# Kernel optimization log

Measured on AMD Instinct MI355X. Metric: run time of the kernel, lower is better.

The kernel has to match this reference:

```python
import jax, jax.numpy as jnp
import numpy as np

IN_DIM = 1024
EMBED = 1024
HEADS = 16
HEAD_DIM = EMBED // HEADS
MAX_LEN = 401


def _sinusoidal_pe(max_len, d_model):
    pos = np.arange(max_len, dtype=np.float32)[:, None]
    div = np.exp(np.arange(0, d_model, 2, dtype=np.float32) * (-np.log(10000.0) / d_model))
    pe = np.zeros((max_len, d_model), dtype=np.float32)
    pe[:, 0::2] = np.sin(pos * div)
    pe[:, 1::2] = np.cos(pos * div)
    return jnp.asarray(pe[None])  # [1, max_len, d]


def setup_inputs() -> dict:
    key = jax.random.key(0)
    ks = jax.random.split(key, 16)
    B, S = 32, 400
    s = 1.0 / np.sqrt(IN_DIM)
    inp = {
        "query": jax.random.normal(ks[0], (B, S, IN_DIM), jnp.float32),
        "key": jax.random.normal(ks[1], (B, S, IN_DIM), jnp.float32),
        "value": jax.random.normal(ks[2], (B, S, IN_DIM), jnp.float32),
        "attn_mask": jnp.zeros((S, S), jnp.float32),
        "pe": _sinusoidal_pe(MAX_LEN, IN_DIM),
        "Wq": jax.random.normal(ks[3], (EMBED, IN_DIM), jnp.float32) * s,
        "bq": jax.random.normal(ks[4], (EMBED,), jnp.float32) * s,
        "Wk": jax.random.normal(ks[5], (EMBED, IN_DIM), jnp.float32) * s,
        "bk": jax.random.normal(ks[6], (EMBED,), jnp.float32) * s,
        "Wv": jax.random.normal(ks[7], (EMBED, IN_DIM), jnp.float32) * s,
        "bv": jax.random.normal(ks[8], (EMBED,), jnp.float32) * s,
        "Wp": jax.random.normal(ks[9], (EMBED, IN_DIM), jnp.float32) * s,
        "bp": jax.random.normal(ks[10], (EMBED,), jnp.float32) * s,
        "Wo": jax.random.normal(ks[11], (IN_DIM, EMBED), jnp.float32) / np.sqrt(EMBED),
        "bo": jax.random.normal(ks[12], (IN_DIM,), jnp.float32) / np.sqrt(EMBED),
        "gates": jax.random.normal(ks[13], (1,), jnp.float32),
    }
    return inp


def reference(query, key, value, attn_mask, pe, Wq, bq, Wk, bk, Wv, bv, Wp, bp, Wo, bo, gates):
    B, Sq, _ = query.shape
    Sk = key.shape[1]
    H, D = HEADS, HEAD_DIM

    pos_q = pe[:, :Sq] @ Wp.T + bp   # [1, Sq, E]
    pos_k = pe[:, :Sk] @ Wp.T + bp   # [1, Sk, E]

    q = (query @ Wq.T + bq + pos_q).reshape(B, Sq, H, D).transpose(0, 2, 1, 3)
    k = (key @ Wk.T + bk + pos_k).reshape(B, Sk, H, D).transpose(0, 2, 1, 3)
    v = (value @ Wv.T + bv + pos_k).reshape(B, Sk, H, D).transpose(0, 2, 1, 3)

    scores = jnp.einsum('bhqd,bhkd->bhqk', q, k) / jnp.sqrt(jnp.float32(D))
    scores = scores + attn_mask[None, None]  # additive mask broadcast over batch/heads
    attn = jax.nn.softmax(scores, axis=-1)   # dropout p=0.0 -> identity

    out = jnp.einsum('bhqk,bhkd->bhqd', attn, v)
    out = out.transpose(0, 2, 1, 3).reshape(B, Sq, H * D)
    return (out @ Wo.T + bo) * gates
```

## Files before the change

kernel.cpp:

```cpp
#include <hip/hip_runtime.h>

typedef __bf16 bf16;
typedef __bf16 bf16x8 __attribute__((ext_vector_type(8)));
typedef __bf16 bf16x4 __attribute__((ext_vector_type(4)));
typedef float f32x4 __attribute__((ext_vector_type(4)));

#define MFMA(a, b, c) __builtin_amdgcn_mfma_f32_16x16x32_bf16(a, b, c, 0, 0, 0)

__device__ __forceinline__ void g2l16(void* lds, const void* g) {
  __builtin_amdgcn_global_load_lds(
      (const __attribute__((address_space(1))) void*)g,
      (__attribute__((address_space(3))) void*)lds, 16, 0, 0);
}

__global__ void cvt_all(
    const float* __restrict__ Wq, const float* __restrict__ Wk, const float* __restrict__ Wv,
    const float* __restrict__ Wo, const float* __restrict__ Wp, const float* __restrict__ pe,
    const float* __restrict__ Xq, const float* __restrict__ Xk, const float* __restrict__ Xv,
    bf16* __restrict__ wqb, bf16* __restrict__ wkb, bf16* __restrict__ wvb,
    bf16* __restrict__ wob, bf16* __restrict__ wpb, bf16* __restrict__ peb,
    bf16* __restrict__ xqb, bf16* __restrict__ xkb, bf16* __restrict__ xvb) {
  int b = blockIdx.x;
  const float* s;
  bf16* d;
  int lb;
  if (b < 5120) {
    int t = b >> 10;
    lb = b & 1023;
    s = (t == 0) ? Wq : (t == 1) ? Wk : (t == 2) ? Wv : (t == 3) ? Wo : Wp;
    d = (t == 0) ? wqb : (t == 1) ? wkb : (t == 2) ? wvb : (t == 3) ? wob : wpb;
  } else if (b < 5520) {
    lb = b - 5120;
    s = pe;
    d = peb;
  } else {
    int bb = b - 5520;
    int t = bb / 12800;
    lb = bb - t * 12800;
    s = (t == 0) ? Xq : (t == 1) ? Xk : Xv;
    d = (t == 0) ? xqb : (t == 1) ? xkb : xvb;
  }
  int i = lb * 256 + threadIdx.x;
  f32x4 v = *(const f32x4*)(s + (size_t)i * 4);
  bf16x4 o;
  o[0] = (bf16)v[0]; o[1] = (bf16)v[1]; o[2] = (bf16)v[2]; o[3] = (bf16)v[3];
  *(bf16x4*)(d + (size_t)i * 4) = o;
}

__global__ __launch_bounds__(256) void gemm_pos(
    const bf16* __restrict__ peb, const bf16* __restrict__ Wpb,
    const float* __restrict__ bp, const float* __restrict__ bq,
    const float* __restrict__ bk, const float* __restrict__ bv,
    bf16* __restrict__ posq, bf16* __restrict__ posk, bf16* __restrict__ posv) {
  __shared__ bf16 smA[128 * 32];
  __shared__ bf16 smB[128 * 32];
  const int mbase = blockIdx.y * 128;
  const int nbase = blockIdx.x * 128;
  const int tid = threadIdx.x;
  const int lane = tid & 63, w = tid >> 6;
  const int wm = (w >> 1) * 64, wn = (w & 1) * 64;
  const int lrow = lane & 15, kg = lane >> 4;
  const f32x4 fz = {0.f, 0.f, 0.f, 0.f};
  f32x4 acc[4][4];
#pragma unroll
  for (int i = 0; i < 4; ++i)
#pragma unroll
    for (int j = 0; j < 4; ++j) acc[i][j] = fz;

  for (int k0 = 0; k0 < 1024; k0 += 32) {
    __syncthreads();
#pragma unroll
    for (int it = 0; it < 2; ++it) {
      int j = it * 256 + tid;
      int r = j >> 2, cl = j & 3;
      int c = cl ^ ((r >> 1) & 3);
      if (mbase + r < 400)
        g2l16(smA + j * 8, peb + (mbase + r) * 1024 + k0 + c * 8);
      else {
        uint4 zz = make_uint4(0, 0, 0, 0);
        *(uint4*)(smA + j * 8) = zz;
      }
    }
#pragma unroll
    for (int it = 0; it < 2; ++it) {
      int j = it * 256 + tid;
      int r = j >> 2, cl = j & 3;
      int c = cl ^ ((r >> 1) & 3);
      g2l16(smB + j * 8, Wpb + (nbase + r) * 1024 + k0 + c * 8);
    }
    __syncthreads();
    bf16x8 af[4], bfr[4];
#pragma unroll
    for (int mt = 0; mt < 4; ++mt) {
      int r = wm + mt * 16 + lrow;
      int ch = kg ^ ((r >> 1) & 3);
      af[mt] = *(const bf16x8*)(smA + r * 32 + ch * 8);
    }
#pragma unroll
    for (int nt = 0; nt < 4; ++nt) {
      int r = wn + nt * 16 + lrow;
      int ch = kg ^ ((r >> 1) & 3);
      bfr[nt] = *(const bf16x8*)(smB + r * 32 + ch * 8);
    }
#pragma unroll
    for (int nt = 0; nt < 4; ++nt)
#pragma unroll
      for (int mt = 0; mt < 4; ++mt)
        acc[mt][nt] = MFMA(af[mt], bfr[nt], acc[mt][nt]);
  }
#pragma unroll
  for (int mt = 0; mt < 4; ++mt)
#pragma unroll
    for (int rg = 0; rg < 4; ++rg) {
      int m = mbase + wm + mt * 16 + kg * 4 + rg;
      if (m < 400) {
#pragma unroll
        for (int nt = 0; nt < 4; ++nt) {
          int n = nbase + wn + nt * 16 + lrow;
          float base = acc[mt][nt][rg] + bp[n];
          posq[m * 1024 + n] = (bf16)(base + bq[n]);
          posk[m * 1024 + n] = (bf16)(base + bk[n]);
          posv[m * 1024 + n] = (bf16)(base + bv[n]);
        }
      }
    }
}

__global__ __launch_bounds__(512, 4) void gemm_qkv(
    const bf16* __restrict__ Xqb, const bf16* __restrict__ Xkb, const bf16* __restrict__ Xvb,
    const bf16* __restrict__ Wqb, const bf16* __restrict__ Wkb, const bf16* __restrict__ Wvb,
    const bf16* __restrict__ posq, const bf16* __restrict__ posk, const bf16* __restrict__ posv,
    bf16* __restrict__ qb, bf16* __restrict__ kbuf, bf16* __restrict__ vt) {
  const int lid = blockIdx.x;
  const int mI = ((lid >> 6) << 3) + (lid & 7);
  const int nI = (lid >> 3) & 7;
  if (mI >= 100) return;
  __shared__ bf16 sm[16384];
  bf16* smA = sm;
  bf16* smB = sm + 8192;
  const int z = blockIdx.y;
  const bf16* X = (z == 0) ? Xqb : (z == 1) ? Xkb : Xvb;
  const bf16* W = (z == 0) ? Wqb : (z == 1) ? Wkb : Wvb;
  const bf16* posz = (z == 0) ? posq : (z == 1) ? posk : posv;
  const int mbase = mI * 128;
  const int nbase = nI * 128;
  const int tid = threadIdx.x;
  const int lane = tid & 63, w = tid >> 6;
  const int wm = (w >> 1) * 32, wn = (w & 1) * 64;
  const int lrow = lane & 15, kg = lane >> 4;
  const f32x4 fz = {0.f, 0.f, 0.f, 0.f};
  f32x4 acc[2][4];
#pragma unroll
  for (int i = 0; i < 2; ++i)
#pragma unroll
    for (int j = 0; j < 4; ++j) acc[i][j] = fz;

  for (int k0 = 0; k0 < 1024; k0 += 64) {
    __syncthreads();
#pragma unroll
    for (int it = 0; it < 2; ++it) {
      int j = it * 512 + tid;
      int r = j >> 3, cl = j & 7;
      g2l16(smA + j * 8, X + (size_t)(mbase + r) * 1024 + k0 + (cl ^ (r & 7)) * 8);
    }
#pragma unroll
    for (int it = 0; it < 2; ++it) {
      int j = it * 512 + tid;
      int r = j >> 3, cl = j & 7;
      g2l16(smB + j * 8, W + (size_t)(nbase + r) * 1024 + k0 + (cl ^ (r & 7)) * 8);
    }
    __syncthreads();
#pragma unroll
    for (int ks = 0; ks < 2; ++ks) {
      bf16x8 af[2], bfr[4];
#pragma unroll
      for (int mt = 0; mt < 2; ++mt) {
        int r = wm + mt * 16 + lrow;
        af[mt] = *(const bf16x8*)(smA + r * 64 + ((ks * 4 + kg) ^ (r & 7)) * 8);
      }
#pragma unroll
      for (int nt = 0; nt < 4; ++nt) {
        int r = wn + nt * 16 + lrow;
        bfr[nt] = *(const bf16x8*)(smB + r * 64 + ((ks * 4 + kg) ^ (r & 7)) * 8);
      }
#pragma unroll
      for (int nt = 0; nt < 4; ++nt)
#pragma unroll
        for (int mt = 0; mt < 2; ++mt)
          acc[mt][nt] = MFMA(af[mt], bfr[nt], acc[mt][nt]);
    }
  }

  if (z < 2) {
    bf16* dst = (z == 0) ? qb : kbuf;
#pragma unroll
    for (int mt = 0; mt < 2; ++mt)
#pragma unroll
      for (int rg = 0; rg < 4; ++rg) {
        int m = mbase + wm + mt * 16 + kg * 4 + rg;
        int bI = m / 400;
        int s = m - bI * 400;
#pragma unroll
        for (int nt = 0; nt < 4; ++nt) {
          int n = nbase + wn + nt * 16 + lrow;
          float v = acc[mt][nt][rg] + (float)posz[s * 1024 + n];
          int h = n >> 6, d = n & 63;
          dst[((size_t)(bI * 16 + h) * 400 + s) * 64 + d] = (bf16)v;
        }
      }
  } else {
    __syncthreads();
    bf16* T = sm;
#pragma unroll
    for (int nt = 0; nt < 4; ++nt) {
      int n = wn + nt * 16 + lrow;
      int ng = nbase + n;
#pragma unroll
      for (int mt = 0; mt < 2; ++mt) {
        int m0 = wm + mt * 16 + kg * 4;
        bf16x4 v4;
#pragma unroll
        for (int rg = 0; rg < 4; ++rg) {
          int m = mbase + m0 + rg;
          int bI = m / 400;
          int s = m - bI * 400;
          v4[rg] = (bf16)(acc[mt][nt][rg] + (float)posz[s * 1024 + ng]);
        }
        int chk = m0 >> 3;
        int st = chk ^ (n & 15);
        *(bf16x4*)(T + n * 128 + st * 8 + (m0 & 7)) = v4;
      }
    }
    __syncthreads();
#pragma unroll
    for (int p = 0; p < 4; ++p) {
      int n = p * 32 + (tid >> 4);
      int chk = tid & 15;
      bf16x8 row = *(const bf16x8*)(T + n * 128 + (chk ^ (n & 15)) * 8);
      int ng = nbase + n;
      int h = ng >> 6, d = ng & 63;
      int m = mbase + chk * 8;
      int bI = m / 400;
      int s = m - bI * 400;
      *(bf16x8*)(vt + ((size_t)(bI * 16 + h) * 64 + d) * 400 + s) = row;
    }
  }
}

__global__ __launch_bounds__(512, 4) void attn_kernel(
    const bf16* __restrict__ qg, const bf16* __restrict__ kg_,
    const bf16* __restrict__ vg, const float* __restrict__ mask,
    bf16* __restrict__ ao) {
  const int lid = blockIdx.x;
  const int qt = (lid >> 3) & 3;
  const int bh = ((lid >> 5) << 3) + (lid & 7);
  __shared__ bf16 smQ[128 * 64];
  __shared__ bf16 smK[128 * 64];
  __shared__ bf16 smV[64 * 128];
  __shared__ bf16 smP[128 * 128];
  const int qbase = qt * 128;
  const int tid = threadIdx.x;
  const int lane = tid & 63;
  const int w = tid >> 6;
  const int lrow = lane & 15, kg = lane >> 4;
  const bf16* Qg = qg + bh * 25600;
  const bf16* Kg = kg_ + bh * 25600;
  const bf16* Vg = vg + bh * 25600;

#pragma unroll
  for (int it = 0; it < 2; ++it) {
    int j = it * 512 + tid;
    int r = j >> 3, cl = j & 7;
    int c = cl ^ (r & 7);
    int s = qbase + r;
    uint4 val = make_uint4(0, 0, 0, 0);
    if (s < 400) val = *(const uint4*)(Qg + s * 64 + c * 8);
    *(uint4*)(smQ + j * 8) = val;
  }

  const f32x4 fz = {0.f, 0.f, 0.f, 0.f};
  f32x4 o[4];
#pragma unroll
  for (int i = 0; i < 4; ++i) o[i] = fz;
  float m_run[4], l_run[4];
  const float* mrow4[4];
#pragma unroll
  for (int i = 0; i < 4; ++i) {
    m_run[i] = -1e30f;
    l_run[i] = 0.f;
    int qs = qbase + w * 16 + kg * 4 + i;
    mrow4[i] = mask + (size_t)((qs < 400) ? qs : 399) * 400;
  }

  for (int kt = 0; kt < 3; ++kt) {
#pragma unroll
    for (int it = 0; it < 2; ++it) {
      int j = it * 512 + tid;
      int r = j >> 3, cl = j & 7;
      int c = cl ^ (r & 7);
      *(uint4*)(smK + j * 8) = *(const uint4*)(Kg + (kt * 128 + r) * 64 + c * 8);
    }
#pragma unroll
    for (int it = 0; it < 2; ++it) {
      int j = it * 512 + tid;
      int r = j >> 4, cl = j & 15;
      int c = cl ^ (r & 15);
      *(uint4*)(smV + j * 8) = *(const uint4*)(Vg + r * 400 + kt * 128 + c * 8);
    }
    __syncthreads();

    f32x4 sc[8];
#pragma unroll
    for (int nt = 0; nt < 8; ++nt) sc[nt] = fz;
    __builtin_amdgcn_s_setprio(1);
#pragma unroll
    for (int ks = 0; ks < 2; ++ks) {
      int rq = w * 16 + lrow;
      int chq = (ks * 4 + kg) ^ (rq & 7);
      bf16x8 aq = *(const bf16x8*)(smQ + rq * 64 + chq * 8);
#pragma unroll
      for (int nt = 0; nt < 8; ++nt) {
        int rk2 = nt * 16 + lrow;
        int chk = (ks * 4 + kg) ^ (rk2 & 7);
        bf16x8 bk8 = *(const bf16x8*)(smK + rk2 * 64 + chk * 8);
        sc[nt] = MFMA(aq, bk8, sc[nt]);
      }
    }
    __builtin_amdgcn_s_setprio(0);

    float alpha[4];
#pragma unroll
    for (int rg = 0; rg < 4; ++rg) {
      const float* mrow = mrow4[rg];
      float rmax = -1e30f;
#pragma unroll
      for (int nt = 0; nt < 8; ++nt) {
        int ksi = kt * 128 + nt * 16 + lrow;
        float v = fmaf(sc[nt][rg], 0.125f, mrow[ksi]);
        sc[nt][rg] = v;
        rmax = fmaxf(rmax, v);
      }
#pragma unroll
      for (int off = 1; off < 16; off <<= 1)
        rmax = fmaxf(rmax, __shfl_xor(rmax, off, 64));
      float mn = fmaxf(m_run[rg], rmax);
      alpha[rg] = __expf(m_run[rg] - mn);
      m_run[rg] = mn;
      float rsum = 0.f;
#pragma unroll
      for (int nt = 0; nt < 8; ++nt) {
        float p = __expf(sc[nt][rg] - mn);
        sc[nt][rg] = p;
        rsum += p;
      }
#pragma unroll
      for (int off = 1; off < 16; off <<= 1)
        rsum += __shfl_xor(rsum, off, 64);
      l_run[rg] = l_run[rg] * alpha[rg] + rsum;
    }
#pragma unroll
    for (int nt2 = 0; nt2 < 4; ++nt2)
#pragma unroll
      for (int rg = 0; rg < 4; ++rg) o[nt2][rg] *= alpha[rg];
#pragma unroll
    for (int nt = 0; nt < 8; ++nt)
#pragma unroll
      for (int rg = 0; rg < 4; ++rg) {
        int row = w * 16 + kg * 4 + rg;
        int col = nt * 16 + lrow;
        int ch = (col >> 3) ^ (row & 15);
        smP[row * 128 + ch * 8 + (col & 7)] = (bf16)sc[nt][rg];
      }
    __syncthreads();
    __builtin_amdgcn_s_setprio(1);
#pragma unroll
    for (int ks2 = 0; ks2 < 4; ++ks2) {
      int rp = w * 16 + lrow;
      int chp = (ks2 * 4 + kg) ^ (rp & 15);
      bf16x8 ap = *(const bf16x8*)(smP + rp * 128 + chp * 8);
#pragma unroll
      for (int nt2 = 0; nt2 < 4; ++nt2) {
        int rv2 = nt2 * 16 + lrow;
        int chv = (ks2 * 4 + kg) ^ (rv2 & 15);
        bf16x8 bv8 = *(const bf16x8*)(smV + rv2 * 128 + chv * 8);
        o[nt2] = MFMA(ap, bv8, o[nt2]);
      }
    }
    __builtin_amdgcn_s_setprio(0);
    __syncthreads();
  }

  {
    if (tid < 128) {
      int r = tid >> 3, cl = tid & 7;
      int c = cl ^ (r & 7);
      *(uint4*)(smK + tid * 8) = *(const uint4*)(Kg + (384 + r) * 64 + c * 8);
    } else if (tid < 256) {
      int t2 = tid - 128;
      int r = t2 >> 1, ci = t2 & 1;
      *(uint4*)(smV + r * 128 + (ci ^ (r & 15)) * 8) =
          *(const uint4*)(Vg + r * 400 + 384 + ci * 8);
    }
    __syncthreads();

    f32x4 sc0 = fz;
    __builtin_amdgcn_s_setprio(1);
#pragma unroll
    for (int ks = 0; ks < 2; ++ks) {
      int rq = w * 16 + lrow;
      int chq = (ks * 4 + kg) ^ (rq & 7);
      bf16x8 aq = *(const bf16x8*)(smQ + rq * 64 + chq * 8);
      int chk = (ks * 4 + kg) ^ (lrow & 7);
      bf16x8 bk8 = *(const bf16x8*)(smK + lrow * 64 + chk * 8);
      sc0 = MFMA(aq, bk8, sc0);
    }
    __builtin_amdgcn_s_setprio(0);

    float alpha[4];
#pragma unroll
    for (int rg = 0; rg < 4; ++rg) {
      float v = fmaf(sc0[rg], 0.125f, mrow4[rg][384 + lrow]);
      float rmax = v;
#pragma unroll
      for (int off = 1; off < 16; off <<= 1)
        rmax = fmaxf(rmax, __shfl_xor(rmax, off, 64));
      float mn = fmaxf(m_run[rg], rmax);
      alpha[rg] = __expf(m_run[rg] - mn);
      m_run[rg] = mn;
      float p = __expf(v - mn);
      sc0[rg] = p;
      float rsum = p;
#pragma unroll
      for (int off = 1; off < 16; off <<= 1)
        rsum += __shfl_xor(rsum, off, 64);
      l_run[rg] = l_run[rg] * alpha[rg] + rsum;
    }
#pragma unroll
    for (int nt2 = 0; nt2 < 4; ++nt2)
#pragma unroll
      for (int rg = 0; rg < 4; ++rg) o[nt2][rg] *= alpha[rg];
#pragma unroll
    for (int rg = 0; rg < 4; ++rg) {
      int row = w * 16 + kg * 4 + rg;
      int ch0 = (lrow >> 3) ^ (row & 15);
      smP[row * 128 + ch0 * 8 + (lrow & 7)] = (bf16)sc0[rg];
      int ch1 = (2 + (lrow >> 3)) ^ (row & 15);
      smP[row * 128 + ch1 * 8 + (lrow & 7)] = (bf16)0.f;
    }
    __syncthreads();
    __builtin_amdgcn_s_setprio(1);
    {
      int rp = w * 16 + lrow;
      int chp = kg ^ (rp & 15);
      bf16x8 ap = *(const bf16x8*)(smP + rp * 128 + chp * 8);
#pragma unroll
      for (int nt2 = 0; nt2 < 4; ++nt2) {
        int rv2 = nt2 * 16 + lrow;
        int chv = kg ^ (rv2 & 15);
        bf16x8 bv8 = *(const bf16x8*)(smV + rv2 * 128 + chv * 8);
        o[nt2] = MFMA(ap, bv8, o[nt2]);
      }
    }
    __builtin_amdgcn_s_setprio(0);
  }

  const int b = bh >> 4, h = bh & 15;
#pragma unroll
  for (int rg = 0; rg < 4; ++rg) {
    int qs = qbase + w * 16 + kg * 4 + rg;
    if (qs < 400) {
      float inv = 1.f / l_run[rg];
#pragma unroll
      for (int nt2 = 0; nt2 < 4; ++nt2) {
        ao[(b * 400 + qs) * 1024 + h * 64 + nt2 * 16 + lrow] =
            (bf16)(o[nt2][rg] * inv);
      }
    }
  }
}

__global__ __launch_bounds__(512, 4) void gemm_out(
    const bf16* __restrict__ aop, const bf16* __restrict__ Wob,
    const float* __restrict__ bo, const float* __restrict__ gates,
    float* __restrict__ out) {
  const int lid = blockIdx.x;
  const int mI = ((lid >> 6) << 3) + (lid & 7);
  const int nI = (lid >> 3) & 7;
  if (mI >= 100) return;
  __shared__ bf16 sm[16384];
  bf16* smA = sm;
  bf16* smB = sm + 8192;
  const int mbase = mI * 128;
  const int nbase = nI * 128;
  const int tid = threadIdx.x;
  const int lane = tid & 63, w = tid >> 6;
  const int wm = (w >> 1) * 32, wn = (w & 1) * 64;
  const int lrow = lane & 15, kg = lane >> 4;
  const float g = gates[0];
  const f32x4 fz = {0.f, 0.f, 0.f, 0.f};
  f32x4 acc[2][4];
#pragma unroll
  for (int i = 0; i < 2; ++i)
#pragma unroll
    for (int j = 0; j < 4; ++j) acc[i][j] = fz;

  for (int k0 = 0; k0 < 1024; k0 += 64) {
    __syncthreads();
#pragma unroll
    for (int it = 0; it < 2; ++it) {
      int j = it * 512 + tid;
      int r = j >> 3, cl = j & 7;
      g2l16(smA + j * 8, aop + (size_t)(mbase + r) * 1024 + k0 + (cl ^ (r & 7)) * 8);
    }
#pragma unroll
    for (int it = 0; it < 2; ++it) {
      int j = it * 512 + tid;
      int r = j >> 3, cl = j & 7;
      g2l16(smB + j * 8, Wob + (size_t)(nbase + r) * 1024 + k0 + (cl ^ (r & 7)) * 8);
    }
    __syncthreads();
#pragma unroll
    for (int ks = 0; ks < 2; ++ks) {
      bf16x8 af[2], bfr[4];
#pragma unroll
      for (int mt = 0; mt < 2; ++mt) {
        int r = wm + mt * 16 + lrow;
        af[mt] = *(const bf16x8*)(smA + r * 64 + ((ks * 4 + kg) ^ (r & 7)) * 8);
      }
#pragma unroll
      for (int nt = 0; nt < 4; ++nt) {
        int r = wn + nt * 16 + lrow;
        bfr[nt] = *(const bf16x8*)(smB + r * 64 + ((ks * 4 + kg) ^ (r & 7)) * 8);
      }
#pragma unroll
      for (int nt = 0; nt < 4; ++nt)
#pragma unroll
        for (int mt = 0; mt < 2; ++mt)
          acc[mt][nt] = MFMA(af[mt], bfr[nt], acc[mt][nt]);
    }
  }
#pragma unroll
  for (int mt = 0; mt < 2; ++mt)
#pragma unroll
    for (int rg = 0; rg < 4; ++rg) {
      int m = mbase + wm + mt * 16 + kg * 4 + rg;
#pragma unroll
      for (int nt = 0; nt < 4; ++nt) {
        int n = nbase + wn + nt * 16 + lrow;
        out[(size_t)m * 1024 + n] = (acc[mt][nt][rg] + bo[n]) * g;
      }
    }
}

extern "C" void kernel_launch(void* const* d_in, const int* in_sizes, int n_in,
                              void* d_out, int out_size, void* d_ws, size_t ws_size,
                              hipStream_t stream) {
  const float* query = (const float*)d_in[0];
  const float* key   = (const float*)d_in[1];
  const float* value = (const float*)d_in[2];
  const float* mask  = (const float*)d_in[3];
  const float* pe    = (const float*)d_in[4];
  const float* Wq = (const float*)d_in[5];
  const float* bq = (const float*)d_in[6];
  const float* Wk = (const float*)d_in[7];
  const float* bk = (const float*)d_in[8];
  const float* Wv = (const float*)d_in[9];
  const float* bv = (const float*)d_in[10];
  const float* Wp = (const float*)d_in[11];
  const float* bp = (const float*)d_in[12];
  const float* Wo = (const float*)d_in[13];
  const float* bo = (const float*)d_in[14];
  const float* gates = (const float*)d_in[15];
  float* out = (float*)d_out;

  char* base = (char*)d_ws;
  size_t off = 0;
  bf16* wq_b = (bf16*)(base + off); off += 2097152;
  bf16* wk_b = (bf16*)(base + off); off += 2097152;
  bf16* wv_b = (bf16*)(base + off); off += 2097152;
  bf16* wo_b = (bf16*)(base + off); off += 2097152;
  bf16* wp_b = (bf16*)(base + off); off += 2097152;
  bf16* pe_b = (bf16*)(base + off); off += 819200;
  bf16* posq = (bf16*)(base + off); off += 819200;
  bf16* posk = (bf16*)(base + off); off += 819200;
  bf16* posv = (bf16*)(base + off); off += 819200;
  bf16* qb = (bf16*)(base + off); off += 26214400;
  bf16* kb = (bf16*)(base + off); off += 26214400;
  bf16* vt = (bf16*)(base + off); off += 26214400;
  bf16* ao = (bf16*)(base + off); off += 26214400;
  bf16* xq_b = ao;
  bf16* xk_b = (bf16*)d_out;
  bf16* xv_b = (bf16*)d_out + 13107200;
  (void)ws_size; (void)in_sizes; (void)n_in; (void)out_size;

  cvt_all<<<43920, 256, 0, stream>>>(Wq, Wk, Wv, Wo, Wp, pe,
                                     query, key, value,
                                     wq_b, wk_b, wv_b, wo_b, wp_b, pe_b,
                                     xq_b, xk_b, xv_b);
  gemm_pos<<<dim3(8, 4), 256, 0, stream>>>(pe_b, wp_b, bp, bq, bk, bv,
                                           posq, posk, posv);
  gemm_qkv<<<dim3(832, 3), 512, 0, stream>>>(xq_b, xk_b, xv_b,
                                             wq_b, wk_b, wv_b,
                                             posq, posk, posv, qb, kb, vt);
  attn_kernel<<<2048, 512, 0, stream>>>(qb, kb, vt, mask, ao);
  gemm_out<<<832, 512, 0, stream>>>(ao, wo_b, bo, gates, out);
}
```

Measured before the change: 524.4 us.

## Shrink attention K/V tiles to 64, keep Q in registers, defer row-sum reduction

Result: slower. 653.3 us (+24.6%).

```diff
diff --git a/kernel.cpp b/kernel.cpp
--- a/kernel.cpp
+++ b/kernel.cpp
@@ -247,17 +247,16 @@
   }
 }
 
-__global__ __launch_bounds__(512, 4) void attn_kernel(
+__global__ __launch_bounds__(512, 8) void attn_kernel(
     const bf16* __restrict__ qg, const bf16* __restrict__ kg_,
     const bf16* __restrict__ vg, const float* __restrict__ mask,
     bf16* __restrict__ ao) {
   const int lid = blockIdx.x;
   const int qt = (lid >> 3) & 3;
   const int bh = ((lid >> 5) << 3) + (lid & 7);
-  __shared__ bf16 smQ[128 * 64];
-  __shared__ bf16 smK[128 * 64];
-  __shared__ bf16 smV[64 * 128];
-  __shared__ bf16 smP[128 * 128];
+  __shared__ bf16 smK[64 * 64];
+  __shared__ bf16 smV[2][64 * 64];
+  __shared__ bf16 smP[128 * 64];
   const int qbase = qt * 128;
   const int tid = threadIdx.x;
   const int lane = tid & 63;
@@ -267,75 +266,62 @@
   const bf16* Kg = kg_ + bh * 25600;
   const bf16* Vg = vg + bh * 25600;
 
-#pragma unroll
-  for (int it = 0; it < 2; ++it) {
-    int j = it * 512 + tid;
-    int r = j >> 3, cl = j & 7;
-    int c = cl ^ (r & 7);
-    int s = qbase + r;
-    uint4 val = make_uint4(0, 0, 0, 0);
-    if (s < 400) val = *(const uint4*)(Qg + s * 64 + c * 8);
-    *(uint4*)(smQ + j * 8) = val;
+  bf16x8 aq[2];
+  {
+    int rq = qbase + w * 16 + lrow;
+    const uint4 zz = make_uint4(0, 0, 0, 0);
+#pragma unroll
+    for (int ks = 0; ks < 2; ++ks) {
+      uint4 v = zz;
+      if (rq < 400) v = *(const uint4*)(Qg + rq * 64 + (ks * 4 + kg) * 8);
+      aq[ks] = *(const bf16x8*)&v;
+    }
   }
 
   const f32x4 fz = {0.f, 0.f, 0.f, 0.f};
   f32x4 o[4];
 #pragma unroll
   for (int i = 0; i < 4; ++i) o[i] = fz;
-  float m_run[4], l_run[4];
-  const float* mrow4[4];
+  float m_run[4], l_part[4];
+  int moff[4];
 #pragma unroll
   for (int i = 0; i < 4; ++i) {
     m_run[i] = -1e30f;
-    l_run[i] = 0.f;
+    l_part[i] = 0.f;
     int qs = qbase + w * 16 + kg * 4 + i;
-    mrow4[i] = mask + (size_t)((qs < 400) ? qs : 399) * 400;
-  }
-
-  for (int kt = 0; kt < 3; ++kt) {
-#pragma unroll
-    for (int it = 0; it < 2; ++it) {
-      int j = it * 512 + tid;
-      int r = j >> 3, cl = j & 7;
-      int c = cl ^ (r & 7);
-      *(uint4*)(smK + j * 8) = *(const uint4*)(Kg + (kt * 128 + r) * 64 + c * 8);
-    }
-#pragma unroll
-    for (int it = 0; it < 2; ++it) {
-      int j = it * 512 + tid;
-      int r = j >> 4, cl = j & 15;
-      int c = cl ^ (r & 15);
-      *(uint4*)(smV + j * 8) = *(const uint4*)(Vg + r * 400 + kt * 128 + c * 8);
-    }
-    __syncthreads();
-
-    f32x4 sc[8];
-#pragma unroll
-    for (int nt = 0; nt < 8; ++nt) sc[nt] = fz;
+    moff[i] = ((qs < 400) ? qs : 399) * 400;
+  }
+  const int stg_r = tid >> 3, stg_c = (tid & 7) ^ (stg_r & 7);
+
+  for (int kt = 0; kt < 6; ++kt) {
+    bf16* Vb = smV[kt & 1];
+    *(uint4*)(smK + tid * 8) =
+        *(const uint4*)(Kg + (kt * 64 + stg_r) * 64 + stg_c * 8);
+    *(uint4*)(Vb + tid * 8) =
+        *(const uint4*)(Vg + stg_r * 400 + kt * 64 + stg_c * 8);
+    __syncthreads();
+
+    f32x4 sc[4];
+#pragma unroll
+    for (int nt = 0; nt < 4; ++nt) sc[nt] = fz;
     __builtin_amdgcn_s_setprio(1);
 #pragma unroll
-    for (int ks = 0; ks < 2; ++ks) {
-      int rq = w * 16 + lrow;
-      int chq = (ks * 4 + kg) ^ (rq & 7);
-      bf16x8 aq = *(const bf16x8*)(smQ + rq * 64 + chq * 8);
-#pragma unroll
-      for (int nt = 0; nt < 8; ++nt) {
-        int rk2 = nt * 16 + lrow;
-        int chk = (ks * 4 + kg) ^ (rk2 & 7);
-        bf16x8 bk8 = *(const bf16x8*)(smK + rk2 * 64 + chk * 8);
-        sc[nt] = MFMA(aq, bk8, sc[nt]);
-      }
-    }
+    for (int ks = 0; ks < 2; ++ks)
+#pragma unroll
+      for (int nt = 0; nt < 4; ++nt) {
+        int rk = nt * 16 + lrow;
+        bf16x8 bk8 = *(const bf16x8*)(smK + rk * 64 + (((ks * 4 + kg) ^ (rk & 7)) * 8));
+        sc[nt] = MFMA(aq[ks], bk8, sc[nt]);
+      }
     __builtin_amdgcn_s_setprio(0);
 
-    float alpha[4];
 #pragma unroll
     for (int rg = 0; rg < 4; ++rg) {
-      const float* mrow = mrow4[rg];
+      const float* mrow = mask + moff[rg];
       float rmax = -1e30f;
 #pragma unroll
-      for (int nt = 0; nt < 8; ++nt) {
-        int ksi = kt * 128 + nt * 16 + lrow;
+      for (int nt = 0; nt < 4; ++nt) {
+        int ksi = kt * 64 + nt * 16 + lrow;
         float v = fmaf(sc[nt][rg], 0.125f, mrow[ksi]);
         sc[nt][rg] = v;
         rmax = fmaxf(rmax, v);
@@ -344,61 +330,54 @@
       for (int off = 1; off < 16; off <<= 1)
         rmax = fmaxf(rmax, __shfl_xor(rmax, off, 64));
       float mn = fmaxf(m_run[rg], rmax);
-      alpha[rg] = __expf(m_run[rg] - mn);
+      float alpha = __expf(m_run[rg] - mn);
       m_run[rg] = mn;
       float rsum = 0.f;
 #pragma unroll
-      for (int nt = 0; nt < 8; ++nt) {
+      for (int nt = 0; nt < 4; ++nt) {
         float p = __expf(sc[nt][rg] - mn);
         sc[nt][rg] = p;
         rsum += p;
       }
-#pragma unroll
-      for (int off = 1; off < 16; off <<= 1)
-        rsum += __shfl_xor(rsum, off, 64);
-      l_run[rg] = l_run[rg] * alpha[rg] + rsum;
-    }
-#pragma unroll
-    for (int nt2 = 0; nt2 < 4; ++nt2)
-#pragma unroll
-      for (int rg = 0; rg < 4; ++rg) o[nt2][rg] *= alpha[rg];
-#pragma unroll
-    for (int nt = 0; nt < 8; ++nt)
+      l_part[rg] = l_part[rg] * alpha + rsum;
+      o[0][rg] *= alpha; o[1][rg] *= alpha; o[2][rg] *= alpha; o[3][rg] *= alpha;
+    }
+#pragma unroll
+    for (int nt = 0; nt < 4; ++nt)
 #pragma unroll
       for (int rg = 0; rg < 4; ++rg) {
         int row = w * 16 + kg * 4 + rg;
         int col = nt * 16 + lrow;
-        int ch = (col >> 3) ^ (row & 15);
-        smP[row * 128 + ch * 8 + (col & 7)] = (bf16)sc[nt][rg];
+        int ch = (col >> 3) ^ (row & 7);
+        smP[row * 64 + ch * 8 + (col & 7)] = (bf16)sc[nt][rg];
       }
     __syncthreads();
     __builtin_amdgcn_s_setprio(1);
 #pragma unroll
-    for (int ks2 = 0; ks2 < 4; ++ks2) {
+    for (int ks2 = 0; ks2 < 2; ++ks2) {
       int rp = w * 16 + lrow;
-      int chp = (ks2 * 4 + kg) ^ (rp & 15);
-      bf16x8 ap = *(const bf16x8*)(smP + rp * 128 + chp * 8);
+      bf16x8 ap = *(const bf16x8*)(smP + rp * 64 + (((ks2 * 4 + kg) ^ (rp & 7)) * 8));
 #pragma unroll
       for (int nt2 = 0; nt2 < 4; ++nt2) {
-        int rv2 = nt2 * 16 + lrow;
-        int chv = (ks2 * 4 + kg) ^ (rv2 & 15);
-        bf16x8 bv8 = *(const bf16x8*)(smV + rv2 * 128 + chv * 8);
+        int rv = nt2 * 16 + lrow;
+        bf16x8 bv8 = *(const bf16x8*)(Vb + rv * 64 + (((ks2 * 4 + kg) ^ (rv & 7)) * 8));
         o[nt2] = MFMA(ap, bv8, o[nt2]);
       }
     }
     __builtin_amdgcn_s_setprio(0);
-    __syncthreads();
   }
 
   {
+    bf16* Vb = smV[0];
+    __syncthreads();
     if (tid < 128) {
       int r = tid >> 3, cl = tid & 7;
-      int c = cl ^ (r & 7);
-      *(uint4*)(smK + tid * 8) = *(const uint4*)(Kg + (384 + r) * 64 + c * 8);
+      *(uint4*)(smK + tid * 8) =
+          *(const uint4*)(Kg + (384 + r) * 64 + (cl ^ (r & 7)) * 8);
     } else if (tid < 256) {
       int t2 = tid - 128;
       int r = t2 >> 1, ci = t2 & 1;
-      *(uint4*)(smV + r * 128 + (ci ^ (r & 15)) * 8) =
+      *(uint4*)(Vb + r * 64 + ((ci ^ (r & 7)) * 8)) =
           *(const uint4*)(Vg + r * 400 + 384 + ci * 8);
     }
     __syncthreads();
@@ -407,57 +386,43 @@
     __builtin_amdgcn_s_setprio(1);
 #pragma unroll
     for (int ks = 0; ks < 2; ++ks) {
-      int rq = w * 16 + lrow;
-      int chq = (ks * 4 + kg) ^ (rq & 7);
-      bf16x8 aq = *(const bf16x8*)(smQ + rq * 64 + chq * 8);
-      int chk = (ks * 4 + kg) ^ (lrow & 7);
-      bf16x8 bk8 = *(const bf16x8*)(smK + lrow * 64 + chk * 8);
-      sc0 = MFMA(aq, bk8, sc0);
+      bf16x8 bk8 = *(const bf16x8*)(smK + lrow * 64 + (((ks * 4 + kg) ^ (lrow & 7)) * 8));
+      sc0 = MFMA(aq[ks], bk8, sc0);
     }
     __builtin_amdgcn_s_setprio(0);
 
-    float alpha[4];
 #pragma unroll
     for (int rg = 0; rg < 4; ++rg) {
-      float v = fmaf(sc0[rg], 0.125f, mrow4[rg][384 + lrow]);
+      float v = fmaf(sc0[rg], 0.125f, mask[moff[rg] + 384 + lrow]);
       float rmax = v;
 #pragma unroll
       for (int off = 1; off < 16; off <<= 1)
         rmax = fmaxf(rmax, __shfl_xor(rmax, off, 64));
       float mn = fmaxf(m_run[rg], rmax);
-      alpha[rg] = __expf(m_run[rg] - mn);
+      float alpha = __expf(m_run[rg] - mn);
       m_run[rg] = mn;
       float p = __expf(v - mn);
       sc0[rg] = p;
-      float rsum = p;
-#pragma unroll
-      for (int off = 1; off < 16; off <<= 1)
-        rsum += __shfl_xor(rsum, off, 64);
-      l_run[rg] = l_run[rg] * alpha[rg] + rsum;
-    }
-#pragma unroll
-    for (int nt2 = 0; nt2 < 4; ++nt2)
-#pragma unroll
-      for (int rg = 0; rg < 4; ++rg) o[nt2][rg] *= alpha[rg];
+      l_part[rg] = l_part[rg] * alpha + p;
+      o[0][rg] *= alpha; o[1][rg] *= alpha; o[2][rg] *= alpha; o[3][rg] *= alpha;
+    }
 #pragma unroll
     for (int rg = 0; rg < 4; ++rg) {
       int row = w * 16 + kg * 4 + rg;
-      int ch0 = (lrow >> 3) ^ (row & 15);
-      smP[row * 128 + ch0 * 8 + (lrow & 7)] = (bf16)sc0[rg];
-      int ch1 = (2 + (lrow >> 3)) ^ (row & 15);
-      smP[row * 128 + ch1 * 8 + (lrow & 7)] = (bf16)0.f;
+      int ch0 = (lrow >> 3) ^ (row & 7);
+      smP[row * 64 + ch0 * 8 + (lrow & 7)] = (bf16)sc0[rg];
+      int ch1 = (2 + (lrow >> 3)) ^ (row & 7);
+      smP[row * 64 + ch1 * 8 + (lrow & 7)] = (bf16)0.f;
     }
     __syncthreads();
     __builtin_amdgcn_s_setprio(1);
     {
       int rp = w * 16 + lrow;
-      int chp = kg ^ (rp & 15);
-      bf16x8 ap = *(const bf16x8*)(smP + rp * 128 + chp * 8);
+      bf16x8 ap = *(const bf16x8*)(smP + rp * 64 + ((kg ^ (rp & 7)) * 8));
 #pragma unroll
       for (int nt2 = 0; nt2 < 4; ++nt2) {
-        int rv2 = nt2 * 16 + lrow;
-        int chv = kg ^ (rv2 & 15);
-        bf16x8 bv8 = *(const bf16x8*)(smV + rv2 * 128 + chv * 8);
+        int rv = nt2 * 16 + lrow;
+        bf16x8 bv8 = *(const bf16x8*)(Vb + rv * 64 + ((kg ^ (rv & 7)) * 8));
         o[nt2] = MFMA(ap, bv8, o[nt2]);
       }
     }
@@ -467,9 +432,13 @@
   const int b = bh >> 4, h = bh & 15;
 #pragma unroll
   for (int rg = 0; rg < 4; ++rg) {
+    float l = l_part[rg];
+#pragma unroll
+    for (int off = 1; off < 16; off <<= 1)
+      l += __shfl_xor(l, off, 64);
     int qs = qbase + w * 16 + kg * 4 + rg;
     if (qs < 400) {
-      float inv = 1.f / l_run[rg];
+      float inv = 1.f / l;
 #pragma unroll
       for (int nt2 = 0; nt2 < 4; ++nt2) {
         ao[(b * 400 + qs) * 1024 + h * 64 + nt2 * 16 + lrow] =
```
